# Optimization experiments

Measured on AMD Instinct MI355X. Metric: run time of the kernel, lower is better.

Reference implementation:

```python
import jax, jax.numpy as jnp
import numpy as np
import math

F_DIM = 512
N_HEADS = 8
HEAD_DIM = F_DIM // N_HEADS
IMG = 16            # image_size
L = IMG ** 3        # voxel sequence length = 4096
PATCH = 196         # patch_number (ViT 14x14)
VIT_RES = 14
RES = 224           # VIEW_IMAGE_RES
SKETCH_DIM = 768
SIGMA = 1.5         # fixed kernel_size (torch draws randomly when None)
GN_GROUPS = 32


def position_encoding(d_model, length):
    pe = np.zeros((length, d_model), dtype=np.float32)
    position = np.arange(length, dtype=np.float32)[:, None]
    div_term = np.exp(np.arange(0, d_model, 2, dtype=np.float32) * -(math.log(10000.0) / d_model))
    pe[:, 0::2] = np.sin(position * div_term)
    pe[:, 1::2] = np.cos(position * div_term)
    return jnp.asarray(pe)


def get_voxel_coordinates(resolution, size=1.0):
    # centers of a resolution^3 grid spanning [-size/2, size/2]
    idx = np.arange(resolution, dtype=np.float32)
    g = np.stack(np.meshgrid(idx, idx, idx, indexing='ij'), -1).reshape(-1, 3)
    return (g + 0.5) / resolution * size - size / 2.0


VOXEL_PE = position_encoding(F_DIM, L)          # (L, F)
COND_PE = position_encoding(F_DIM, PATCH)       # (S, F)
VOXEL_PTS = jnp.asarray(get_voxel_coordinates(IMG))  # (L, 3)
_vg = np.arange(VIT_RES, dtype=np.float32)
VIT_PIXELS = jnp.asarray(np.stack(np.meshgrid(_vg, _vg, indexing='ij'), -1).reshape(PATCH, 2))  # (S, 2)


def setup_inputs() -> dict:
    key = jax.random.key(0)
    ks = jax.random.split(key, 12)
    B = 8
    s = 0.02
    return {
        'x': jax.random.normal(ks[0], (B, F_DIM, IMG, IMG, IMG), jnp.float32),
        'sketch_feature': jax.random.normal(ks[1], (B, PATCH, SKETCH_DIM), jnp.float32),
        'projection_matrix': jax.random.normal(ks[2], (B, 1, 3, 3), jnp.float32),
        'gn_scale': jnp.ones((F_DIM,), jnp.float32),
        'gn_bias': jnp.zeros((F_DIM,), jnp.float32),
        'conv_w': jax.random.normal(ks[3], (F_DIM, F_DIM, 3, 3, 3), jnp.float32) * s,
        'conv_b': jnp.zeros((F_DIM,), jnp.float32),
        'k_w': jax.random.normal(ks[4], (F_DIM, SKETCH_DIM), jnp.float32) * s,
        'k_b': jnp.zeros((F_DIM,), jnp.float32),
        'v_w': jax.random.normal(ks[5], (F_DIM, SKETCH_DIM), jnp.float32) * s,
        'v_b': jnp.zeros((F_DIM,), jnp.float32),
        'in_proj_w': jax.random.normal(ks[6], (3 * F_DIM, F_DIM), jnp.float32) * s,
        'in_proj_b': jnp.zeros((3 * F_DIM,), jnp.float32),
        'out_w': jax.random.normal(ks[7], (F_DIM, F_DIM), jnp.float32) * s,
        'out_b': jnp.zeros((F_DIM,), jnp.float32),
    }


def _group_norm(x, scale, bias, groups=GN_GROUPS, eps=1e-5):
    B, C = x.shape[0], x.shape[1]
    xr = x.reshape(B, groups, C // groups, -1)
    m = xr.mean(axis=(2, 3), keepdims=True)
    v = xr.var(axis=(2, 3), keepdims=True)
    xn = ((xr - m) / jnp.sqrt(v + eps)).reshape(x.shape)
    shp = (1, C) + (1,) * (x.ndim - 2)
    return xn * scale.reshape(shp) + bias.reshape(shp)


def _attn_mask(projection_matrix):
    # project voxel centers, clamp to pixel grid, threshold cdist to vit patch centers
    P = projection_matrix[:, 0]                                  # (B,3,3)
    pc = jnp.einsum('bij,nj->bni', P, VOXEL_PTS)                 # (B,L,3)
    pixels = pc[..., 0:2] / pc[..., 2:3]
    pixels = jnp.clip(jnp.round(pixels), 0.0, RES - 1.0)         # clamp_pixel
    x_idx = (2.0 * pixels[..., 1:2] + 1.0) / RES * VIT_RES / 2.0
    y_idx = (2.0 * (RES - 1.0 - pixels[..., 0:1]) + 1.0) / RES * VIT_RES / 2.0
    ps = jnp.concatenate([x_idx, y_idx], -1) - 0.5               # (B,L,2)
    dist = jnp.linalg.norm(ps[:, :, None, :] - VIT_PIXELS[None, None], axis=-1)  # (B,L,S)
    return jnp.abs(dist) > (SIGMA - 1e-6)                        # True = masked out


def _forward(x, sketch_feature, projection_matrix, gn_scale, gn_bias, conv_w, conv_b,
             k_w, k_b, v_w, v_b, in_proj_w, in_proj_b, out_w, out_b):
    B = x.shape[0]
    # q path: GroupNorm -> SiLU -> Conv3d(3, pad 1)
    h = jax.nn.silu(_group_norm(x, gn_scale, gn_bias))
    h = jax.lax.conv_general_dilated(h, conv_w, window_strides=(1, 1, 1),
                                     padding=[(1, 1)] * 3,
                                     dimension_numbers=('NCDHW', 'OIDHW', 'NCDHW'))
    h = h + conv_b.reshape(1, F_DIM, 1, 1, 1)
    q = h.reshape(B, F_DIM, L).transpose(0, 2, 1) + VOXEL_PE[None]        # (B,L,F)

    mask = _attn_mask(projection_matrix)                                   # (B,L,S)

    k = sketch_feature @ k_w.T + k_b + COND_PE[None]                       # (B,S,F)
    v = sketch_feature @ v_w.T + v_b + COND_PE[None]

    # nn.MultiheadAttention (eval: no dropout)
    wq, wk, wv = jnp.split(in_proj_w, 3, axis=0)
    bq, bk, bv = jnp.split(in_proj_b, 3, axis=0)
    qh = (q @ wq.T + bq).reshape(B, L, N_HEADS, HEAD_DIM).transpose(0, 2, 1, 3)
    kh = (k @ wk.T + bk).reshape(B, PATCH, N_HEADS, HEAD_DIM).transpose(0, 2, 1, 3)
    vh = (v @ wv.T + bv).reshape(B, PATCH, N_HEADS, HEAD_DIM).transpose(0, 2, 1, 3)

    scores = jnp.einsum('bhld,bhsd->bhls', qh, kh) / math.sqrt(HEAD_DIM)   # (B,H,L,S)
    scores = jnp.where(mask[:, None], -jnp.inf, scores)                    # mask shared over heads
    attn = jax.nn.softmax(scores, axis=-1)
    o = jnp.einsum('bhls,bhsd->bhld', attn, vh)
    o = o.transpose(0, 2, 1, 3).reshape(B, L, F_DIM)
    o = o @ out_w.T + out_b                                                # (B,L,F)
    return o.transpose(0, 2, 1).reshape(B, F_DIM, IMG, IMG, IMG)


def reference(x, sketch_feature, projection_matrix, gn_scale, gn_bias, conv_w, conv_b,
              k_w, k_b, v_w, v_b, in_proj_w, in_proj_b, out_w, out_b):
    return _forward(x, sketch_feature, projection_matrix, gn_scale, gn_bias, conv_w, conv_b,
                    k_w, k_b, v_w, v_b, in_proj_w, in_proj_b, out_w, out_b)
```

## Files before the change

kernel.cpp:

```cpp
#include <hip/hip_runtime.h>

#define DEV static __device__ __forceinline__

typedef unsigned short u16;
typedef unsigned int u32;
typedef unsigned long long u64;
typedef float f32x4 __attribute__((ext_vector_type(4)));
typedef short bfrag __attribute__((ext_vector_type(8)));

#define FD 512
#define LV 4096
#define PV 5832

DEV float b2f(u16 u){ union{ u32 i; float f; } x; x.i = ((u32)u)<<16; return x.f; }
DEV u16 f2b(float f){ union{ float f; u32 i; } x; x.f = f; u32 r = x.i; r += 0x7fffu + ((r>>16)&1u); return (u16)(r>>16); }

DEV void g2l(const void* g, void* s){
  __builtin_amdgcn_global_load_lds((const __attribute__((address_space(1))) void*)g,
                                   (__attribute__((address_space(3))) void*)s, 16, 0, 0);
}

static const size_t o_wt  = 0;
static const size_t o_wq  = 14155776;
static const size_t o_ow  = 14680064;
static const size_t o_vpe = 15204352;
static const size_t o_cpe = 23592960;
static const size_t o_gn  = 23994368;
static const size_t o_mask= 23996416;
static const size_t o_khb = 25044992;
static const size_t o_vhb = 26748928;
static const size_t o_hp  = 36841472;
static const size_t o_qb  = 84617216;
static const size_t o_qh  = 118171648;
static const size_t o_skb = o_qh;
static const size_t o_kwb = o_qh + 2555904;
static const size_t o_vwb = o_qh + 3342336;
static const size_t o_wkb = o_qh + 4128768;
static const size_t o_wvb = o_qh + 4653056;
static const size_t o_ktb = o_qh + 5177344;
static const size_t o_vtb = o_qh + 6881280;

__global__ __launch_bounds__(256) void prep_all(const float* __restrict__ convw,
    const float* __restrict__ ipw, const float* __restrict__ ow,
    const float* __restrict__ sketch, const float* __restrict__ kw, const float* __restrict__ vw,
    u16* __restrict__ wt, u16* __restrict__ Wq, u16* __restrict__ Ow, u16* __restrict__ Skb,
    u16* __restrict__ Kwb, u16* __restrict__ Vwb, u16* __restrict__ Wkb, u16* __restrict__ Wvb){
  int blk = blockIdx.x, t = threadIdx.x;
  if (blk < 1024){
    int idx = blk*256 + t;
    const float* src = convw + (size_t)idx*27;
    float v[27];
    #pragma unroll
    for (int k=0;k<27;k++) v[k] = src[k];
    #pragma unroll
    for (int k=0;k<27;k++) wt[(size_t)k*262144 + idx] = f2b(v[k]);
  } else if (blk < 2048){ int i=(blk-1024)*256+t;  Wq[i]  = f2b(ipw[i]); }
  else if (blk < 3072){   int i=(blk-2048)*256+t;  Ow[i]  = f2b(ow[i]); }
  else if (blk < 7776){   int i=(blk-3072)*256+t;  if (i<1204224) Skb[i] = f2b(sketch[i]); }
  else if (blk < 9312){   int i=(blk-7776)*256+t;  Kwb[i] = f2b(kw[i]); }
  else if (blk < 10848){  int i=(blk-9312)*256+t;  Vwb[i] = f2b(vw[i]); }
  else if (blk < 11872){  int i=(blk-10848)*256+t; Wkb[i] = f2b(ipw[262144+i]); }
  else {                  int i=(blk-11872)*256+t; Wvb[i] = f2b(ipw[524288+i]); }
}

__global__ __launch_bounds__(256) void geom_prep(float* __restrict__ vpe, float* __restrict__ cpe,
    const float* __restrict__ proj, u64* __restrict__ maskb){
  int blk = blockIdx.x, t = threadIdx.x;
  if (blk < 4292){
    float* pe = (blk < 4096) ? vpe : cpe;
    int l = (blk < 4096) ? blk : blk - 4096;
    const float fac = -0.017988946039015984f;
    float dt = expf((float)(2*t) * fac);
    float ang = (float)l * dt;
    pe[(size_t)l*FD + 2*t]     = sinf(ang);
    pe[(size_t)l*FD + 2*t + 1] = cosf(ang);
    return;
  }
  int idx = (blk-4292)*256 + t;
  int b = idx >> 12, v = idx & 4095;
  float P[9];
  #pragma unroll
  for (int j=0;j<9;j++) P[j] = proj[b*9 + j];
  int zi=v>>8, yi=(v>>4)&15, xi=v&15;
  float pt0 = ((float)zi + 0.5f)/16.0f - 0.5f;
  float pt1 = ((float)yi + 0.5f)/16.0f - 0.5f;
  float pt2 = ((float)xi + 0.5f)/16.0f - 0.5f;
  float pc0 = __fadd_rn(__fadd_rn(__fmul_rn(P[0],pt0), __fmul_rn(P[1],pt1)), __fmul_rn(P[2],pt2));
  float pc1 = __fadd_rn(__fadd_rn(__fmul_rn(P[3],pt0), __fmul_rn(P[4],pt1)), __fmul_rn(P[5],pt2));
  float pc2 = __fadd_rn(__fadd_rn(__fmul_rn(P[6],pt0), __fmul_rn(P[7],pt1)), __fmul_rn(P[8],pt2));
  float r0 = __fdiv_rn(pc0, pc2);
  float r1 = __fdiv_rn(pc1, pc2);
  float px0 = fminf(fmaxf(rintf(r0), 0.f), 223.f);
  float px1 = fminf(fmaxf(rintf(r1), 0.f), 223.f);
  float x_idx = __fmul_rn(__fdiv_rn(__fadd_rn(__fmul_rn(2.f,px1),1.f), 224.f), 14.f) * 0.5f;
  float y_idx = __fmul_rn(__fdiv_rn(__fadd_rn(__fmul_rn(2.f,__fadd_rn(223.f,-px0)),1.f), 224.f), 14.f) * 0.5f;
  float ps0 = __fadd_rn(x_idx, -0.5f);
  float ps1 = __fadd_rn(y_idx, -0.5f);
  const float TH = 1.4999990463256836f;
  u64 abits[4] = {0,0,0,0};
  #pragma unroll 1
  for (int s=0;s<196;s++){
    int si = s/14, sj = s - si*14;
    float d0 = __fadd_rn(ps0, -(float)si);
    float d1 = __fadd_rn(ps1, -(float)sj);
    float dist = sqrtf(__fadd_rn(__fmul_rn(d0,d0), __fmul_rn(d1,d1)));
    if (!(fabsf(dist) > TH)) abits[s>>6] |= (1ull << (s&63));
  }
  u64* out = maskb + (size_t)idx*4;
  out[0]=abits[0]; out[1]=abits[1]; out[2]=abits[2]; out[3]=abits[3];
}

__global__ __launch_bounds__(256) void gn_stats(const float* __restrict__ x, float* __restrict__ stats){
  int bg = blockIdx.x;
  const float* base = x + (size_t)bg*65536;
  float s=0.f, q=0.f;
  for (int i=threadIdx.x;i<65536;i+=256){ float v = base[i]; s+=v; q+=v*v; }
  #pragma unroll
  for (int off=32; off>0; off>>=1){ s += __shfl_xor(s,off); q += __shfl_xor(q,off); }
  __shared__ float red[8];
  int w = threadIdx.x>>6;
  if ((threadIdx.x&63)==0){ red[w*2]=s; red[w*2+1]=q; }
  __syncthreads();
  if (threadIdx.x==0){
    float S=red[0]+red[2]+red[4]+red[6];
    float Q=red[1]+red[3]+red[5]+red[7];
    float m = S*(1.f/65536.f);
    float var = Q*(1.f/65536.f) - m*m;
    stats[bg] = m;
    stats[256+bg] = rsqrtf(var + 1e-5f);
  }
}

__global__ __launch_bounds__(256) void gn_apply_b(const float* __restrict__ x,
    const float* __restrict__ stats, const float* __restrict__ sc, const float* __restrict__ bi,
    u16* __restrict__ hp){
  int zb = blockIdx.x, cb = blockIdx.y, b = blockIdx.z;
  const float* xb = x + (size_t)b*FD*LV;
  u16* hpb = hp + (size_t)b*PV*FD;
  int t = threadIdx.x;
  int y = t>>4, xx = t&15;
  size_t hrow = ((size_t)(zb+1)*324 + (size_t)(y+1)*18 + (xx+1))*FD;
  int v = zb*256 + t;
  #pragma unroll 4
  for (int cc=0; cc<64; ++cc){
    int c = cb*64 + cc;
    float val = xb[(size_t)c*LV + v];
    int g = c>>4;
    float m = stats[b*32+g];
    float r = stats[256 + b*32+g];
    float xn = (val - m)*r*sc[c] + bi[c];
    hpb[hrow + c] = f2b(xn / (1.f + expf(-xn)));
  }
}

__global__ __launch_bounds__(256,4) void conv_mfma(const u16* __restrict__ hp,
    const u16* __restrict__ wt, const float* __restrict__ cbias,
    const float* __restrict__ vpe, u16* __restrict__ qb){
  __shared__ __align__(16) u16 Al[8192];
  __shared__ __align__(16) u16 Wl[8192];
  int tid = threadIdx.x;
  int w = tid>>6, l = tid&63;
  int v0 = blockIdx.x*128, n0 = blockIdx.y*128, b = blockIdx.z;
  int swz = ((l&7) ^ ((l>>3)&7))*8;
  size_t abase[4], wbase[4];
  #pragma unroll
  for (int j=0;j<4;j++){
    int r = w*32 + j*8 + (l>>3);
    int v = v0 + r;
    int z = v>>8, yy=(v>>4)&15, xx=v&15;
    abase[j] = ((size_t)b*PV + (size_t)(z*324 + yy*18 + xx))*FD + swz;
    wbase[j] = (size_t)(n0 + r)*FD + swz;
  }
  f32x4 zero4 = {0.f,0.f,0.f,0.f};
  f32x4 acc[4][4];
  #pragma unroll
  for (int i=0;i<4;i++)
    #pragma unroll
    for (int j=0;j<4;j++) acc[i][j] = zero4;
  int wr = (w>>1)*64, wc = (w&1)*64;
  for (int kk=0; kk<216; ++kk){
    int off = kk>>3;
    int ks  = (kk&7)<<6;
    int dz = off/9; int rem = off - dz*9; int dy = rem/3; int dx = rem - dy*3;
    size_t adelta = (size_t)(dz*324 + dy*18 + dx)*FD + ks;
    size_t wdelta = (size_t)off*262144 + ks;
    #pragma unroll
    for (int j=0;j<4;j++){
      g2l(hp + abase[j] + adelta, Al + (w*32 + j*8)*64);
      g2l(wt + wbase[j] + wdelta, Wl + (w*32 + j*8)*64);
    }
    __syncthreads();
    #pragma unroll
    for (int ks2=0; ks2<2; ++ks2){
      bfrag af[4], wf[4];
      #pragma unroll
      for (int i=0;i<4;i++){
        int ra = wr + i*16 + (l&15);
        af[i] = *(const bfrag*)(Al + ra*64 + (((ks2<<2) + (l>>4)) ^ (l&7))*8);
        int rb = wc + i*16 + (l&15);
        wf[i] = *(const bfrag*)(Wl + rb*64 + (((ks2<<2) + (l>>4)) ^ (l&7))*8);
      }
      #pragma unroll
      for (int i=0;i<4;i++)
        #pragma unroll
        for (int j=0;j<4;j++)
          acc[i][j] = __builtin_amdgcn_mfma_f32_16x16x32_bf16(af[i], wf[j], acc[i][j], 0,0,0);
    }
    __syncthreads();
  }
  #pragma unroll
  for (int i=0;i<4;i++)
    #pragma unroll
    for (int j=0;j<4;j++)
      #pragma unroll
      for (int rg=0;rg<4;rg++){
        int row = wr + i*16 + ((l>>4)<<2) + rg;
        int col = wc + j*16 + (l&15);
        int v = v0 + row, n = n0 + col;
        float cv = acc[i][j][rg] + cbias[n] + vpe[(size_t)v*FD + n];
        qb[((size_t)b*LV + v)*FD + n] = f2b(cv);
      }
}

template<bool TRANS>
__global__ __launch_bounds__(256,2) void gemm_mfma(const u16* __restrict__ A, const u16* __restrict__ W,
    const float* __restrict__ bias, void* __restrict__ Cout){
  __shared__ __align__(16) u16 Al[4096];
  __shared__ __align__(16) u16 Wl[4096];
  int tid = threadIdx.x;
  int w = tid>>6, l = tid&63;
  int m0 = blockIdx.x*128, n0 = blockIdx.y*128, b = blockIdx.z;
  int sw_src = (((l&3) ^ ((l>>3)&3)))*8;
  int sw_rd  = (((l>>4) ^ ((l>>1)&3)))*8;
  size_t abase[2], wbase[2];
  #pragma unroll
  for (int j=0;j<2;j++){
    int r = (w*2+j)*16 + (l>>2);
    abase[j] = ((size_t)b*LV + m0 + r)*FD + sw_src;
    wbase[j] = (size_t)(n0 + r)*FD + sw_src;
  }
  f32x4 zero4 = {0.f,0.f,0.f,0.f};
  f32x4 acc[4][4];
  #pragma unroll
  for (int i=0;i<4;i++)
    #pragma unroll
    for (int j=0;j<4;j++) acc[i][j] = zero4;
  int wr = (w>>1)*64, wc = (w&1)*64;
  for (int k0=0; k0<512; k0+=32){
    #pragma unroll
    for (int j=0;j<2;j++){
      g2l(A + abase[j] + k0, Al + (w*2+j)*512);
      g2l(W + wbase[j] + k0, Wl + (w*2+j)*512);
    }
    __syncthreads();
    bfrag af[4], wf[4];
    #pragma unroll
    for (int i=0;i<4;i++){
      int r  = wr + i*16 + (l&15);
      af[i] = *(const bfrag*)(Al + r*32 + sw_rd);
      int cn = wc + i*16 + (l&15);
      wf[i] = *(const bfrag*)(Wl + cn*32 + sw_rd);
    }
    #pragma unroll
    for (int i=0;i<4;i++)
      #pragma unroll
      for (int j=0;j<4;j++)
        acc[i][j] = __builtin_amdgcn_mfma_f32_16x16x32_bf16(af[i], wf[j], acc[i][j], 0,0,0);
    __syncthreads();
  }
  #pragma unroll
  for (int i=0;i<4;i++)
    #pragma unroll
    for (int j=0;j<4;j++){
      if constexpr (TRANS){
        int row = m0 + wr + i*16 + ((l>>4)<<2);
        int col = n0 + wc + j*16 + (l&15);
        float bv = bias[col];
        float4 val = { acc[i][j][0]+bv, acc[i][j][1]+bv, acc[i][j][2]+bv, acc[i][j][3]+bv };
        *(float4*)&(((float*)Cout)[((size_t)b*FD + col)*LV + row]) = val;
      } else {
        #pragma unroll
        for (int rg=0;rg<4;rg++){
          int row = m0 + wr + i*16 + ((l>>4)<<2) + rg;
          int col = n0 + wc + j*16 + (l&15);
          ((u16*)Cout)[((size_t)b*LV + row)*FD + col] = f2b(acc[i][j][rg] + bias[col]);
        }
      }
    }
}

template<bool ADDPE>
__global__ __launch_bounds__(256,2) void gemm_kv(const u16* __restrict__ A0, const u16* __restrict__ A1,
    const u16* __restrict__ W0, const u16* __restrict__ W1,
    const float* __restrict__ b0, const float* __restrict__ b1,
    const float* __restrict__ pe, u16* __restrict__ C0, u16* __restrict__ C1, int K){
  const u16* A = blockIdx.z ? A1 : A0;
  const u16* W = blockIdx.z ? W1 : W0;
  const float* bias = blockIdx.z ? b1 : b0;
  u16* Cout = blockIdx.z ? C1 : C0;
  __shared__ __align__(16) u16 Al[4096];
  __shared__ __align__(16) u16 Wl[4096];
  int tid = threadIdx.x;
  int w = tid>>6, l = tid&63;
  int m0 = blockIdx.x*128, n0 = blockIdx.y*128;
  int sw_src = (((l&3) ^ ((l>>3)&3)))*8;
  int sw_rd  = (((l>>4) ^ ((l>>1)&3)))*8;
  size_t abase[2], wbase[2];
  #pragma unroll
  for (int j=0;j<2;j++){
    int r = (w*2+j)*16 + (l>>2);
    abase[j] = (size_t)(m0 + r)*K + sw_src;
    wbase[j] = (size_t)(n0 + r)*K + sw_src;
  }
  f32x4 zero4 = {0.f,0.f,0.f,0.f};
  f32x4 acc[4][4];
  #pragma unroll
  for (int i=0;i<4;i++)
    #pragma unroll
    for (int j=0;j<4;j++) acc[i][j] = zero4;
  int wr = (w>>1)*64, wc = (w&1)*64;
  for (int k0=0; k0<K; k0+=32){
    #pragma unroll
    for (int j=0;j<2;j++){
      g2l(A + abase[j] + k0, Al + (w*2+j)*512);
      g2l(W + wbase[j] + k0, Wl + (w*2+j)*512);
    }
    __syncthreads();
    bfrag af[4], wf[4];
    #pragma unroll
    for (int i=0;i<4;i++){
      int r  = wr + i*16 + (l&15);
      af[i] = *(const bfrag*)(Al + r*32 + sw_rd);
      int cn = wc + i*16 + (l&15);
      wf[i] = *(const bfrag*)(Wl + cn*32 + sw_rd);
    }
    #pragma unroll
    for (int i=0;i<4;i++)
      #pragma unroll
      for (int j=0;j<4;j++)
        acc[i][j] = __builtin_amdgcn_mfma_f32_16x16x32_bf16(af[i], wf[j], acc[i][j], 0,0,0);
    __syncthreads();
  }
  #pragma unroll
  for (int i=0;i<4;i++)
    #pragma unroll
    for (int j=0;j<4;j++)
      #pragma unroll
      for (int rg=0;rg<4;rg++){
        int row = m0 + wr + i*16 + ((l>>4)<<2) + rg;
        int col = n0 + wc + j*16 + (l&15);
        float cv = acc[i][j][rg] + bias[col];
        if constexpr (ADDPE) cv += pe[(size_t)(row % 196)*FD + col];
        Cout[(size_t)row*FD + col] = f2b(cv);
      }
}

__global__ __launch_bounds__(256) void attn_lit(const u16* __restrict__ qh,
    const u16* __restrict__ khb, const u16* __restrict__ vhb,
    const u64* __restrict__ maskb, u16* __restrict__ obuf){
  int v = blockIdx.x*256 + threadIdx.x;
  int h = blockIdx.y, b = blockIdx.z;
  const u64* mrow = maskb + ((size_t)b*LV + v)*4;
  u64 abits[4] = {mrow[0], mrow[1], mrow[2], mrow[3]};

  float qr[64];
  {
    const uint4* qp = (const uint4*)(qh + ((size_t)b*LV + v)*FD + h*64);
    #pragma unroll
    for (int c=0;c<8;c++){
      uint4 u = qp[c];
      qr[c*8+0]=b2f((u16)(u.x&0xffffu)); qr[c*8+1]=b2f((u16)(u.x>>16));
      qr[c*8+2]=b2f((u16)(u.y&0xffffu)); qr[c*8+3]=b2f((u16)(u.y>>16));
      qr[c*8+4]=b2f((u16)(u.z&0xffffu)); qr[c*8+5]=b2f((u16)(u.z>>16));
      qr[c*8+6]=b2f((u16)(u.w&0xffffu)); qr[c*8+7]=b2f((u16)(u.w>>16));
    }
  }
  const u16* kb = khb + (size_t)(b*196)*FD + h*64;
  const u16* vb = vhb + (size_t)(b*196)*FD + h*64;
  float o[64];
  #pragma unroll
  for (int d=0;d<64;d++) o[d]=0.f;
  float ssum = 0.f;
  for (int s=0;s<196;s++){
    if (!((abits[s>>6] >> (s&63)) & 1ull)) continue;
    const uint4* kr = (const uint4*)(kb + (size_t)s*FD);
    float dot = 0.f;
    #pragma unroll
    for (int c=0;c<8;c++){
      uint4 u = kr[c];
      dot += qr[c*8+0]*b2f((u16)(u.x&0xffffu)) + qr[c*8+1]*b2f((u16)(u.x>>16))
           + qr[c*8+2]*b2f((u16)(u.y&0xffffu)) + qr[c*8+3]*b2f((u16)(u.y>>16))
           + qr[c*8+4]*b2f((u16)(u.z&0xffffu)) + qr[c*8+5]*b2f((u16)(u.z>>16))
           + qr[c*8+6]*b2f((u16)(u.w&0xffffu)) + qr[c*8+7]*b2f((u16)(u.w>>16));
    }
    float e = expf(dot*0.125f);
    ssum += e;
    const uint4* vr = (const uint4*)(vb + (size_t)s*FD);
    #pragma unroll
    for (int c=0;c<8;c++){
      uint4 u = vr[c];
      o[c*8+0] += e*b2f((u16)(u.x&0xffffu)); o[c*8+1] += e*b2f((u16)(u.x>>16));
      o[c*8+2] += e*b2f((u16)(u.y&0xffffu)); o[c*8+3] += e*b2f((u16)(u.y>>16));
      o[c*8+4] += e*b2f((u16)(u.z&0xffffu)); o[c*8+5] += e*b2f((u16)(u.z>>16));
      o[c*8+6] += e*b2f((u16)(u.w&0xffffu)); o[c*8+7] += e*b2f((u16)(u.w>>16));
    }
  }
  float inv = (ssum > 0.f) ? 1.f/ssum : 0.f;
  u32* op = (u32*)(obuf + ((size_t)b*LV + v)*FD + h*64);
  #pragma unroll
  for (int c=0;c<32;c++){
    u32 lo = f2b(o[c*2]*inv);
    u32 hi = f2b(o[c*2+1]*inv);
    op[c] = lo | (hi<<16);
  }
}

extern "C" void kernel_launch(void* const* d_in, const int* in_sizes, int n_in,
                              void* d_out, int out_size, void* d_ws, size_t ws_size,
                              hipStream_t stream) {
  (void)in_sizes; (void)n_in; (void)out_size; (void)ws_size;
  const float* x_in  = (const float*)d_in[0];
  const float* sketch= (const float*)d_in[1];
  const float* projm = (const float*)d_in[2];
  const float* gnsc  = (const float*)d_in[3];
  const float* gnbi  = (const float*)d_in[4];
  const float* convw = (const float*)d_in[5];
  const float* convb = (const float*)d_in[6];
  const float* kw_in = (const float*)d_in[7];
  const float* kb_in = (const float*)d_in[8];
  const float* vw_in = (const float*)d_in[9];
  const float* vb_in = (const float*)d_in[10];
  const float* ipw   = (const float*)d_in[11];
  const float* ipb   = (const float*)d_in[12];
  const float* ow_in = (const float*)d_in[13];
  const float* ob_in = (const float*)d_in[14];
  char* ws = (char*)d_ws;
  u16*   wt   = (u16*)(ws + o_wt);
  u16*   Wq   = (u16*)(ws + o_wq);
  u16*   Ow   = (u16*)(ws + o_ow);
  float* vpe  = (float*)(ws + o_vpe);
  float* cpe  = (float*)(ws + o_cpe);
  float* stats= (float*)(ws + o_gn);
  u64*   maskb= (u64*)(ws + o_mask);
  u16*   khb  = (u16*)(ws + o_khb);
  u16*   vhb  = (u16*)(ws + o_vhb);
  u16*   hp   = (u16*)(ws + o_hp);
  u16*   qb   = (u16*)(ws + o_qb);
  u16*   qhb  = (u16*)(ws + o_qh);
  u16*   Skb  = (u16*)(ws + o_skb);
  u16*   Kwb  = (u16*)(ws + o_kwb);
  u16*   Vwb  = (u16*)(ws + o_vwb);
  u16*   Wkb  = (u16*)(ws + o_wkb);
  u16*   Wvb  = (u16*)(ws + o_wvb);
  u16*   ktb  = (u16*)(ws + o_ktb);
  u16*   vtb  = (u16*)(ws + o_vtb);
  u16*   obuf = qb;

  hipMemsetAsync(hp, 0, 47775744, stream);
  hipMemsetAsync((char*)Skb + 2408448, 0, 147456, stream);
  prep_all<<<12896,256,0,stream>>>(convw, ipw, ow_in, sketch, kw_in, vw_in,
                                   wt, Wq, Ow, Skb, Kwb, Vwb, Wkb, Wvb);
  geom_prep<<<4420,256,0,stream>>>(vpe, cpe, projm, maskb);
  gn_stats<<<256,256,0,stream>>>(x_in, stats);
  gemm_kv<true ><<<dim3(13,4,2),256,0,stream>>>(Skb, Skb, Kwb, Vwb, kb_in, vb_in, cpe, ktb, vtb, 768);
  gemm_kv<false><<<dim3(13,4,2),256,0,stream>>>(ktb, vtb, Wkb, Wvb, ipb+512, ipb+1024, nullptr, khb, vhb, 512);

  gn_apply_b<<<dim3(16,8,8),256,0,stream>>>(x_in, stats, gnsc, gnbi, hp);
  conv_mfma<<<dim3(32,4,8),256,0,stream>>>(hp, wt, convb, vpe, qb);
  gemm_mfma<false><<<dim3(32,4,8),256,0,stream>>>(qb, Wq, ipb, qhb);
  attn_lit<<<dim3(16,8,8),256,0,stream>>>(qhb, khb, vhb, maskb, obuf);
  gemm_mfma<true ><<<dim3(32,4,8),256,0,stream>>>(obuf, Ow, ob_in, d_out);
}
```

Measured before the change: 775.0 us.

## Rewrite cross-attention with bf16 MFMA tiles and a transposed V buffer

Replaces the per-thread scalar attention loop, where each thread walks all 196 keys for one query and head, with a block-tiled version built on bf16 MFMA. QK^T scores are computed from K staged in LDS, masked and exponentiated into a P tile in LDS, and multiplied by a transposed V. The V projection GEMM epilogue now also writes that transposed, padded V layout so the PV product can read contiguous fragments. The aim is to move the attention math from scalar FP32 ALU onto matrix cores. In exchange, P is rounded to bf16, and the unwritten padding in the transposed V buffer is relied on being multiplied only by zero probabilities.

```diff
diff --git a/kernel.cpp b/kernel.cpp
--- a/kernel.cpp
+++ b/kernel.cpp
@@ -11,6 +11,8 @@
 #define FD 512
 #define LV 4096
 #define PV 5832
+#define SVT 224
+#define SP  228
 
 DEV float b2f(u16 u){ union{ u32 i; float f; } x; x.i = ((u32)u)<<16; return x.f; }
 DEV u16 f2b(float f){ union{ float f; u32 i; } x; x.f = f; u32 r = x.i; r += 0x7fffu + ((r>>16)&1u); return (u16)(r>>16); }
@@ -29,6 +31,7 @@
 static const size_t o_mask= 23996416;
 static const size_t o_khb = 25044992;
 static const size_t o_vhb = 26748928;
+static const size_t o_vt  = 28452864;
 static const size_t o_hp  = 36841472;
 static const size_t o_qb  = 84617216;
 static const size_t o_qh  = 118171648;
@@ -293,7 +296,8 @@
 __global__ __launch_bounds__(256,2) void gemm_kv(const u16* __restrict__ A0, const u16* __restrict__ A1,
     const u16* __restrict__ W0, const u16* __restrict__ W1,
     const float* __restrict__ b0, const float* __restrict__ b1,
-    const float* __restrict__ pe, u16* __restrict__ C0, u16* __restrict__ C1, int K){
+    const float* __restrict__ pe, u16* __restrict__ C0, u16* __restrict__ C1,
+    u16* __restrict__ vt, int K){
   const u16* A = blockIdx.z ? A1 : A0;
   const u16* W = blockIdx.z ? W1 : W0;
   const float* bias = blockIdx.z ? b1 : b0;
@@ -351,67 +355,105 @@
         int col = n0 + wc + j*16 + (l&15);
         float cv = acc[i][j][rg] + bias[col];
         if constexpr (ADDPE) cv += pe[(size_t)(row % 196)*FD + col];
-        Cout[(size_t)row*FD + col] = f2b(cv);
+        u16 cb16 = f2b(cv);
+        Cout[(size_t)row*FD + col] = cb16;
+        if (vt && blockIdx.z){
+          int bb = row / 196;
+          if (bb < 8){
+            int s = row - bb*196;
+            vt[((size_t)(bb*512) + col)*SVT + s] = cb16;
+          }
+        }
       }
 }
 
-__global__ __launch_bounds__(256) void attn_lit(const u16* __restrict__ qh,
-    const u16* __restrict__ khb, const u16* __restrict__ vhb,
+__global__ __launch_bounds__(256,2) void attn_mfma(const u16* __restrict__ qh,
+    const u16* __restrict__ khb, const u16* __restrict__ vT,
     const u64* __restrict__ maskb, u16* __restrict__ obuf){
-  int v = blockIdx.x*256 + threadIdx.x;
-  int h = blockIdx.y, b = blockIdx.z;
-  const u64* mrow = maskb + ((size_t)b*LV + v)*4;
-  u64 abits[4] = {mrow[0], mrow[1], mrow[2], mrow[3]};
-
-  float qr[64];
+  __shared__ __align__(16) u16 Ks[208*64];
+  __shared__ __align__(16) u16 P[64*SP];
+  int tid = threadIdx.x, w = tid>>6, l = tid&63;
+  int v0 = blockIdx.x*64, h = blockIdx.y, b = blockIdx.z;
+
   {
-    const uint4* qp = (const uint4*)(qh + ((size_t)b*LV + v)*FD + h*64);
-    #pragma unroll
-    for (int c=0;c<8;c++){
-      uint4 u = qp[c];
-      qr[c*8+0]=b2f((u16)(u.x&0xffffu)); qr[c*8+1]=b2f((u16)(u.x>>16));
-      qr[c*8+2]=b2f((u16)(u.y&0xffffu)); qr[c*8+3]=b2f((u16)(u.y>>16));
-      qr[c*8+4]=b2f((u16)(u.z&0xffffu)); qr[c*8+5]=b2f((u16)(u.z>>16));
-      qr[c*8+6]=b2f((u16)(u.w&0xffffu)); qr[c*8+7]=b2f((u16)(u.w>>16));
-    }
-  }
-  const u16* kb = khb + (size_t)(b*196)*FD + h*64;
-  const u16* vb = vhb + (size_t)(b*196)*FD + h*64;
-  float o[64];
-  #pragma unroll
-  for (int d=0;d<64;d++) o[d]=0.f;
-  float ssum = 0.f;
-  for (int s=0;s<196;s++){
-    if (!((abits[s>>6] >> (s&63)) & 1ull)) continue;
-    const uint4* kr = (const uint4*)(kb + (size_t)s*FD);
-    float dot = 0.f;
-    #pragma unroll
-    for (int c=0;c<8;c++){
-      uint4 u = kr[c];
-      dot += qr[c*8+0]*b2f((u16)(u.x&0xffffu)) + qr[c*8+1]*b2f((u16)(u.x>>16))
-           + qr[c*8+2]*b2f((u16)(u.y&0xffffu)) + qr[c*8+3]*b2f((u16)(u.y>>16))
-           + qr[c*8+4]*b2f((u16)(u.z&0xffffu)) + qr[c*8+5]*b2f((u16)(u.z>>16))
-           + qr[c*8+6]*b2f((u16)(u.w&0xffffu)) + qr[c*8+7]*b2f((u16)(u.w>>16));
-    }
-    float e = expf(dot*0.125f);
-    ssum += e;
-    const uint4* vr = (const uint4*)(vb + (size_t)s*FD);
-    #pragma unroll
-    for (int c=0;c<8;c++){
-      uint4 u = vr[c];
-      o[c*8+0] += e*b2f((u16)(u.x&0xffffu)); o[c*8+1] += e*b2f((u16)(u.x>>16));
-      o[c*8+2] += e*b2f((u16)(u.y&0xffffu)); o[c*8+3] += e*b2f((u16)(u.y>>16));
-      o[c*8+4] += e*b2f((u16)(u.z&0xffffu)); o[c*8+5] += e*b2f((u16)(u.z>>16));
-      o[c*8+6] += e*b2f((u16)(u.w&0xffffu)); o[c*8+7] += e*b2f((u16)(u.w>>16));
-    }
-  }
-  float inv = (ssum > 0.f) ? 1.f/ssum : 0.f;
-  u32* op = (u32*)(obuf + ((size_t)b*LV + v)*FD + h*64);
-  #pragma unroll
-  for (int c=0;c<32;c++){
-    u32 lo = f2b(o[c*2]*inv);
-    u32 hi = f2b(o[c*2+1]*inv);
-    op[c] = lo | (hi<<16);
+    const u16* khbase = khb + ((size_t)(b*196))*FD + h*64;
+    int row8 = l>>3, ch = l&7;
+    #pragma unroll
+    for (int j=0;j<7;j++){
+      int g = w + j*4;
+      if (g < 26){
+        int s = g*8 + row8;
+        g2l(khbase + (size_t)s*FD + ((ch ^ (row8&7))<<3), Ks + g*512);
+      }
+    }
+  }
+  bfrag aq[2];
+  {
+    const u16* qbase = qh + ((size_t)(b*LV) + v0 + w*16 + (l&15))*FD + h*64 + ((l>>4)<<3);
+    aq[0] = *(const bfrag*)(qbase);
+    aq[1] = *(const bfrag*)(qbase + 32);
+  }
+  u64 mw[4][4];
+  #pragma unroll
+  for (int rg=0;rg<4;rg++){
+    int vv = v0 + w*16 + ((l>>4)<<2) + rg;
+    const u64* mr = maskb + ((size_t)(b*LV) + vv)*4;
+    mw[rg][0]=mr[0]; mw[rg][1]=mr[1]; mw[rg][2]=mr[2]; mw[rg][3]=mr[3];
+  }
+  __syncthreads();
+
+  float rsum[4] = {0.f,0.f,0.f,0.f};
+  #pragma unroll 1
+  for (int nt=0; nt<13; ++nt){
+    f32x4 accs = {0.f,0.f,0.f,0.f};
+    int sN = nt*16 + (l&15);
+    #pragma unroll
+    for (int ks=0;ks<2;ks++){
+      bfrag bk = *(const bfrag*)(Ks + sN*64 + ((((ks<<2)+(l>>4)) ^ (l&7))<<3));
+      accs = __builtin_amdgcn_mfma_f32_16x16x32_bf16(aq[ks], bk, accs, 0,0,0);
+    }
+    int q = sN>>6, bitpos = sN&63;
+    #pragma unroll
+    for (int rg=0;rg<4;rg++){
+      float e = ((mw[rg][q]>>bitpos)&1ull) ? __expf(accs[rg]*0.125f) : 0.f;
+      rsum[rg] += e;
+      P[(size_t)(w*16 + ((l>>4)<<2) + rg)*SP + sN] = f2b(e);
+    }
+  }
+  {
+    int r = w*16 + (l>>2);
+    int c0 = 208 + (l&3)*4;
+    #pragma unroll
+    for (int c=0;c<4;c++) P[(size_t)r*SP + c0 + c] = 0;
+  }
+  #pragma unroll
+  for (int rg=0;rg<4;rg++){
+    float s = rsum[rg];
+    s += __shfl_xor(s,1); s += __shfl_xor(s,2); s += __shfl_xor(s,4); s += __shfl_xor(s,8);
+    rsum[rg] = s;
+  }
+
+  const u16* vbase = vT + ((size_t)(b*FD) + h*64)*SVT;
+  f32x4 acco[4];
+  #pragma unroll
+  for (int dt=0;dt<4;dt++){ f32x4 z={0.f,0.f,0.f,0.f}; acco[dt]=z; }
+  #pragma unroll 1
+  for (int ks=0;ks<7;ks++){
+    bfrag ap = *(const bfrag*)(P + (size_t)(w*16 + (l&15))*SP + ks*32 + ((l>>4)<<3));
+    #pragma unroll
+    for (int dt=0;dt<4;dt++){
+      bfrag bv = *(const bfrag*)(vbase + (size_t)(dt*16 + (l&15))*SVT + ks*32 + ((l>>4)<<3));
+      acco[dt] = __builtin_amdgcn_mfma_f32_16x16x32_bf16(ap, bv, acco[dt], 0,0,0);
+    }
+  }
+  #pragma unroll
+  for (int rg=0;rg<4;rg++){
+    int vv = v0 + w*16 + ((l>>4)<<2) + rg;
+    float inv = (rsum[rg] > 0.f) ? 1.f/rsum[rg] : 0.f;
+    #pragma unroll
+    for (int dt=0;dt<4;dt++){
+      obuf[((size_t)(b*LV) + vv)*FD + h*64 + dt*16 + (l&15)] = f2b(acco[dt][rg]*inv);
+    }
   }
 }
 
@@ -444,6 +486,7 @@
   u64*   maskb= (u64*)(ws + o_mask);
   u16*   khb  = (u16*)(ws + o_khb);
   u16*   vhb  = (u16*)(ws + o_vhb);
+  u16*   vt   = (u16*)(ws + o_vt);
   u16*   hp   = (u16*)(ws + o_hp);
   u16*   qb   = (u16*)(ws + o_qb);
   u16*   qhb  = (u16*)(ws + o_qh);
@@ -462,12 +505,12 @@
                                    wt, Wq, Ow, Skb, Kwb, Vwb, Wkb, Wvb);
   geom_prep<<<4420,256,0,stream>>>(vpe, cpe, projm, maskb);
   gn_stats<<<256,256,0,stream>>>(x_in, stats);
-  gemm_kv<true ><<<dim3(13,4,2),256,0,stream>>>(Skb, Skb, Kwb, Vwb, kb_in, vb_in, cpe, ktb, vtb, 768);
-  gemm_kv<false><<<dim3(13,4,2),256,0,stream>>>(ktb, vtb, Wkb, Wvb, ipb+512, ipb+1024, nullptr, khb, vhb, 512);
+  gemm_kv<true ><<<dim3(13,4,2),256,0,stream>>>(Skb, Skb, Kwb, Vwb, kb_in, vb_in, cpe, ktb, vtb, nullptr, 768);
+  gemm_kv<false><<<dim3(13,4,2),256,0,stream>>>(ktb, vtb, Wkb, Wvb, ipb+512, ipb+1024, nullptr, khb, vhb, vt, 512);
 
   gn_apply_b<<<dim3(16,8,8),256,0,stream>>>(x_in, stats, gnsc, gnbi, hp);
   conv_mfma<<<dim3(32,4,8),256,0,stream>>>(hp, wt, convb, vpe, qb);
   gemm_mfma<false><<<dim3(32,4,8),256,0,stream>>>(qb, Wq, ipb, qhb);
-  attn_lit<<<dim3(16,8,8),256,0,stream>>>(qhb, khb, vhb, maskb, obuf);
+  attn_mfma<<<dim3(64,8,8),256,0,stream>>>(qhb, khb, vt, maskb, obuf);
   gemm_mfma<true ><<<dim3(32,4,8),256,0,stream>>>(obuf, Ow, ob_in, d_out);
 }
```

New measurement: 810.3 us. +4.5%, slower.
